# Optimization experiments

Measured on AMD Instinct MI355X. Metric: run time of the kernel, lower is better.

The kernel has to match this reference:

```python
import jax, jax.numpy as jnp
import numpy as np

B, S, F = 256, 512, 26
H, M, C = 512, 256, 20  # rnn_hidden, mlp_hidden, num_classes


def setup_inputs() -> dict:
    key = jax.random.key(0)
    ks = jax.random.split(key, 9)
    s_ih = 1.0 / np.sqrt(H)
    return {
        "x": jax.random.normal(ks[0], (B, S, F), dtype=jnp.float32),
        "w_ih": jax.random.uniform(ks[1], (4 * H, F), jnp.float32, -s_ih, s_ih),
        "w_hh": jax.random.uniform(ks[2], (4 * H, H), jnp.float32, -s_ih, s_ih),
        "b_ih": jax.random.uniform(ks[3], (4 * H,), jnp.float32, -s_ih, s_ih),
        "b_hh": jax.random.uniform(ks[4], (4 * H,), jnp.float32, -s_ih, s_ih),
        "w1": jax.random.uniform(ks[5], (M, H), jnp.float32, -s_ih, s_ih),
        "b1": jax.random.uniform(ks[6], (M,), jnp.float32, -s_ih, s_ih),
        "w2": jax.random.uniform(ks[7], (C, M), jnp.float32, -1.0 / np.sqrt(M), 1.0 / np.sqrt(M)),
        "b2": jax.random.uniform(ks[8], (C,), jnp.float32, -1.0 / np.sqrt(M), 1.0 / np.sqrt(M)),
    }


def reference(x, w_ih, w_hh, b_ih, b_hh, w1, b1, w2, b2):
    b, s, _ = x.shape
    h0 = jnp.zeros((b, H), x.dtype)
    c0 = jnp.zeros((b, H), x.dtype)
    bias = b_ih + b_hh

    def step(carry, xt):
        h, c = carry
        # original stores hx.data -> state carried into next step is detached
        h = jax.lax.stop_gradient(h)
        c = jax.lax.stop_gradient(c)
        z = xt @ w_ih.T + h @ w_hh.T + bias  # [b, 4H]
        i, f, g, o = jnp.split(z, 4, axis=-1)  # PyTorch gate order i,f,g,o
        c2 = jax.nn.sigmoid(f) * c + jax.nn.sigmoid(i) * jnp.tanh(g)
        h2 = jax.nn.sigmoid(o) * jnp.tanh(c2)
        return (h2, c2), h2

    _, hs = jax.lax.scan(step, (h0, c0), jnp.transpose(x, (1, 0, 2)))  # hs: [s, b, H]
    hs = jnp.transpose(hs, (1, 0, 2))  # [b, s, H]
    hidden = jax.nn.relu(jnp.einsum("bsh,mh->bsm", hs, w1) + b1)
    logits = jnp.einsum("bsm,cm->bsc", hidden, w2) + b2
    return jax.nn.log_softmax(logits, axis=-1)
```

## Files before the change

kernel.cpp:

```cpp
#include <hip/hip_runtime.h>

#define S_LEN 512
#define HID   512
#define FEAT  26
#define NCLS  20
#define DRING 16

typedef short bf16x8 __attribute__((ext_vector_type(8)));
typedef float f32x4  __attribute__((ext_vector_type(4)));

__device__ __forceinline__ unsigned short f2bf(float f) {
    unsigned u = __builtin_bit_cast(unsigned, f);
    unsigned r = (u + 0x7FFFu + ((u >> 16) & 1u)) >> 16;
    return (unsigned short)r;
}
__device__ __forceinline__ float sigm(float x) { return 1.f / (1.f + __expf(-x)); }
__device__ __forceinline__ float tanh_f(float x) {
    float xc = fminf(fmaxf(x, -15.f), 15.f);
    float t = __expf(-2.f * xc);
    return (1.f - t) / (1.f + t);
}

__device__ __forceinline__ void load4_coherent(const unsigned short* p,
                                               uint4& a0, uint4& a1, uint4& a2, uint4& a3) {
    asm volatile(
        "global_load_dwordx4 %0, %4, off sc0 sc1\n\t"
        "global_load_dwordx4 %1, %5, off sc0 sc1\n\t"
        "global_load_dwordx4 %2, %6, off sc0 sc1\n\t"
        "global_load_dwordx4 %3, %7, off sc0 sc1\n\t"
        "s_waitcnt vmcnt(0)"
        : "=&v"(a0), "=&v"(a1), "=&v"(a2), "=&v"(a3)
        : "v"(p), "v"(p + 8), "v"(p + 16), "v"(p + 24)
        : "memory");
}
__device__ __forceinline__ void store_coherent(unsigned short* p, unsigned d) {
    asm volatile(
        "global_store_dword %0, %1, off sc0 sc1\n\t"
        "s_waitcnt vmcnt(0)"
        :: "v"(p), "v"(d) : "memory");
}
__device__ __forceinline__ void store_coherent_x2(unsigned short* p, unsigned long long d) {
    asm volatile(
        "global_store_dwordx2 %0, %1, off sc0 sc1\n\t"
        "s_waitcnt vmcnt(0)"
        :: "v"(p), "v"(d) : "memory");
}
__device__ __forceinline__ void store_u32_nowait(unsigned* p, unsigned d) {
    asm volatile("global_store_dword %0, %1, off sc0 sc1" :: "v"(p), "v"(d) : "memory");
}
__device__ __forceinline__ unsigned load_u32_coherent(const unsigned* p) {
    unsigned v;
    asm volatile("global_load_dword %0, %1, off sc0 sc1\n\ts_waitcnt vmcnt(0)"
                 : "=v"(v) : "v"(p) : "memory");
    return v;
}

__global__ void prep_kernel(const float* __restrict__ w1, const float* __restrict__ w2,
                            unsigned short* __restrict__ w1b, unsigned short* __restrict__ w2b,
                            unsigned* __restrict__ syncw, int nclear) {
    int i = blockIdx.x * 256 + threadIdx.x;
    if (i < nclear) syncw[i] = 0u;
    if (i < 256 * 512) w1b[i] = f2bf(w1[i]);
    if (i < NCLS * 256) w2b[i] = f2bf(w2[i]);
}

__global__ __launch_bounds__(256, 1) void lstm_big_kernel(
    const float* __restrict__ x,
    const float* __restrict__ w_ih,
    const float* __restrict__ w_hh,
    const float* __restrict__ b_ih,
    const float* __restrict__ b_hh,
    const unsigned short* __restrict__ w1b,
    const float* __restrict__ b1,
    const unsigned short* __restrict__ w2b,
    const float* __restrict__ b2,
    float* __restrict__ out,
    unsigned short* __restrict__ hs,
    unsigned* __restrict__ flags)
{
    const int tid  = threadIdx.x;
    const int wave = tid >> 6;
    const int lane = tid & 63;
    const int quad = lane >> 4;
    const int l16  = lane & 15;
    const int wg   = blockIdx.x;

    __shared__ __align__(16) unsigned short At[16 * 552];
    __shared__ float zb[16 * 260];
    __shared__ __align__(16) unsigned short hid[16 * 264];
    __shared__ float lg[16 * 24];
    __shared__ unsigned rdy;
    if (tid == 0) rdy = 0u;
    __syncthreads();

    if (wg < 128) {
        const int clust = wg >> 3;
        const int wic   = wg & 7;
        const int B0    = clust * 16;
        const int U0    = wic * 64;

        bf16x8 bB[4][17];
#pragma unroll
        for (int tl = 0; tl < 4; ++tl) {
            const int row = wave * 512 + U0 + tl * 16 + l16;
            const float* wrow = w_hh + (size_t)row * HID;
#pragma unroll
            for (int kk = 0; kk < 16; ++kk) {
                const float* p = wrow + kk * 32 + quad * 8;
                bf16x8 v;
#pragma unroll
                for (int j = 0; j < 8; ++j) v[j] = (short)f2bf(p[j]);
                bB[tl][kk] = v;
            }
            const float* irow = w_ih + (size_t)row * FEAT;
            bf16x8 v;
#pragma unroll
            for (int j = 0; j < 8; ++j) {
                int ftr = quad * 8 + j;
                v[j] = (ftr < FEAT) ? (short)f2bf(irow[ftr]) : (short)0;
            }
            bB[tl][16] = v;
        }

        const int gb = tid >> 4;
        const int gu = tid & 15;
        float bias[4][4];
#pragma unroll
        for (int uu = 0; uu < 4; ++uu)
#pragma unroll
            for (int g = 0; g < 4; ++g) {
                int r = g * 512 + U0 + 4 * gu + uu;
                bias[uu][g] = b_ih[r] + b_hh[r];
            }
        float cst[4] = {0.f, 0.f, 0.f, 0.f};

        const int sm = tid >> 4;
        const int sc = tid & 15;
        unsigned short* hsc = hs + (size_t)clust * S_LEN * 16 * HID;
        unsigned* myflag = flags + (clust * 8 + wic) * 16;
        const unsigned* peer = flags + (clust * 8 + (lane & 7)) * 16;

        for (int t = 0; t < S_LEN; ++t) {
            {
                unsigned pk = 0u;
                if (sc <= 12) {
                    float2 xv = *(const float2*)(x + ((size_t)(B0 + sm) * S_LEN + t) * FEAT + sc * 2);
                    pk = (unsigned)f2bf(xv.x) | ((unsigned)f2bf(xv.y) << 16);
                }
                *(unsigned*)(At + sm * 552 + 512 + sc * 2) = pk;
            }
            if (t > 0) {
                if (wave == 0) {
                    for (;;) {
                        unsigned v = load_u32_coherent(peer);
                        if (__ballot(v >= (unsigned)t) == ~0ull) break;
                        __builtin_amdgcn_s_sleep(1);
                    }
                    if (lane == 0)
                        __hip_atomic_store(&rdy, (unsigned)t, __ATOMIC_RELAXED,
                                           __HIP_MEMORY_SCOPE_WORKGROUP);
                } else {
                    while (__hip_atomic_load(&rdy, __ATOMIC_RELAXED,
                                             __HIP_MEMORY_SCOPE_WORKGROUP) < (unsigned)t)
                        __builtin_amdgcn_s_sleep(1);
                }
                const unsigned short* src =
                    hsc + ((size_t)(t - 1) * 16 + sm) * HID + sc * 32;
                unsigned short* dst = At + sm * 552 + sc * 32;
                uint4 a0, a1, a2, a3;
                load4_coherent(src, a0, a1, a2, a3);
                *(uint4*)(dst)      = a0;
                *(uint4*)(dst + 8)  = a1;
                *(uint4*)(dst + 16) = a2;
                *(uint4*)(dst + 24) = a3;
            }
            __syncthreads();

            f32x4 acc[4];
#pragma unroll
            for (int tl = 0; tl < 4; ++tl) acc[tl] = (f32x4){0.f, 0.f, 0.f, 0.f};
            const unsigned short* arow = At + l16 * 552 + quad * 8;
            if (t > 0) {
#pragma unroll
                for (int kk = 0; kk < 17; ++kk) {
                    bf16x8 a = __builtin_bit_cast(bf16x8, *(const uint4*)(arow + kk * 32));
#pragma unroll
                    for (int tl = 0; tl < 4; ++tl)
                        acc[tl] = __builtin_amdgcn_mfma_f32_16x16x32_bf16(a, bB[tl][kk], acc[tl], 0, 0, 0);
                }
            } else {
                bf16x8 a = __builtin_bit_cast(bf16x8, *(const uint4*)(arow + 16 * 32));
#pragma unroll
                for (int tl = 0; tl < 4; ++tl)
                    acc[tl] = __builtin_amdgcn_mfma_f32_16x16x32_bf16(a, bB[tl][16], acc[tl], 0, 0, 0);
            }
#pragma unroll
            for (int tl = 0; tl < 4; ++tl)
#pragma unroll
                for (int r = 0; r < 4; ++r)
                    zb[(quad * 4 + r) * 260 + wave * 64 + tl * 16 + l16] = acc[tl][r];
            __syncthreads();

            {
                const float* zrow = zb + gb * 260;
                unsigned short hv[4];
#pragma unroll
                for (int uu = 0; uu < 4; ++uu) {
                    int u = 4 * gu + uu;
                    float zi = zrow[u]       + bias[uu][0];
                    float zf = zrow[64 + u]  + bias[uu][1];
                    float zg = zrow[128 + u] + bias[uu][2];
                    float zo = zrow[192 + u] + bias[uu][3];
                    float cn = sigm(zf) * cst[uu] + sigm(zi) * tanh_f(zg);
                    cst[uu] = cn;
                    hv[uu] = f2bf(sigm(zo) * tanh_f(cn));
                }
                unsigned long long d = (unsigned long long)hv[0]
                                     | ((unsigned long long)hv[1] << 16)
                                     | ((unsigned long long)hv[2] << 32)
                                     | ((unsigned long long)hv[3] << 48);
                unsigned short* hp = hsc + ((size_t)t * 16 + gb) * HID + U0 + 4 * gu;
                store_coherent_x2(hp, d);
            }
            __syncthreads();
            if (tid == 0) store_u32_nowait(myflag, (unsigned)(t + 1));
        }
    } else {
        const int mwg  = wg - 128;
        const int mc   = mwg >> 3;
        const int m    = mwg & 7;
        const int B0   = mc * 16;
        const unsigned* peer = flags + (mc * 8 + (lane & 7)) * 16;
        const unsigned short* hsc = hs + (size_t)mc * S_LEN * 16 * HID;
        const int sm = tid >> 4;
        const int sc = tid & 15;

        for (int t = m; t < S_LEN; t += 8) {
            if (wave == 0) {
                for (;;) {
                    unsigned v = load_u32_coherent(peer);
                    if (__ballot(v >= (unsigned)(t + 1)) == ~0ull) break;
                    __builtin_amdgcn_s_sleep(8);
                }
                if (lane == 0)
                    __hip_atomic_store(&rdy, (unsigned)(t + 1), __ATOMIC_RELAXED,
                                       __HIP_MEMORY_SCOPE_WORKGROUP);
            } else {
                while (__hip_atomic_load(&rdy, __ATOMIC_RELAXED,
                                         __HIP_MEMORY_SCOPE_WORKGROUP) < (unsigned)(t + 1))
                    __builtin_amdgcn_s_sleep(8);
            }
            {
                const unsigned short* src = hsc + ((size_t)t * 16 + sm) * HID + sc * 32;
                unsigned short* dst = At + sm * 552 + sc * 32;
                uint4 a0, a1, a2, a3;
                load4_coherent(src, a0, a1, a2, a3);
                *(uint4*)(dst)      = a0;
                *(uint4*)(dst + 8)  = a1;
                *(uint4*)(dst + 16) = a2;
                *(uint4*)(dst + 24) = a3;
            }
            __syncthreads();

            f32x4 a1[4];
#pragma unroll
            for (int nt = 0; nt < 4; ++nt) a1[nt] = (f32x4){0.f, 0.f, 0.f, 0.f};
#pragma unroll
            for (int kk = 0; kk < 16; ++kk) {
                bf16x8 a = __builtin_bit_cast(
                    bf16x8, *(const uint4*)(At + l16 * 552 + kk * 32 + quad * 8));
#pragma unroll
                for (int nt = 0; nt < 4; ++nt) {
                    int n = wave * 64 + nt * 16 + l16;
                    bf16x8 b = __builtin_bit_cast(
                        bf16x8, *(const uint4*)(w1b + (size_t)n * 512 + kk * 32 + quad * 8));
                    a1[nt] = __builtin_amdgcn_mfma_f32_16x16x32_bf16(a, b, a1[nt], 0, 0, 0);
                }
            }
#pragma unroll
            for (int nt = 0; nt < 4; ++nt) {
                int n = wave * 64 + nt * 16 + l16;
                float bv = b1[n];
#pragma unroll
                for (int r = 0; r < 4; ++r)
                    hid[(quad * 4 + r) * 264 + n] = f2bf(fmaxf(a1[nt][r] + bv, 0.f));
            }
            __syncthreads();
            if (wave == 0) {
                f32x4 a2[2];
                a2[0] = (f32x4){0.f, 0.f, 0.f, 0.f};
                a2[1] = (f32x4){0.f, 0.f, 0.f, 0.f};
#pragma unroll
                for (int kk = 0; kk < 8; ++kk) {
                    bf16x8 a = __builtin_bit_cast(
                        bf16x8, *(const uint4*)(hid + l16 * 264 + kk * 32 + quad * 8));
#pragma unroll
                    for (int nt = 0; nt < 2; ++nt) {
                        int n = nt * 16 + l16;
                        bf16x8 b;
                        if (n < NCLS) {
                            b = __builtin_bit_cast(
                                bf16x8, *(const uint4*)(w2b + (size_t)n * 256 + kk * 32 + quad * 8));
                        } else {
                            uint4 z; z.x = z.y = z.z = z.w = 0u;
                            b = __builtin_bit_cast(bf16x8, z);
                        }
                        a2[nt] = __builtin_amdgcn_mfma_f32_16x16x32_bf16(a, b, a2[nt], 0, 0, 0);
                    }
                }
#pragma unroll
                for (int nt = 0; nt < 2; ++nt) {
                    int n = nt * 16 + l16;
                    if (n < NCLS) {
                        float bv = b2[n];
#pragma unroll
                        for (int r = 0; r < 4; ++r)
                            lg[(quad * 4 + r) * 24 + n] = a2[nt][r] + bv;
                    }
                }
            }
            __syncthreads();
            if (tid < 16) {
                float v[NCLS];
                float mx = -3.4e38f;
#pragma unroll
                for (int c = 0; c < NCLS; ++c) { v[c] = lg[tid * 24 + c]; mx = fmaxf(mx, v[c]); }
                float s = 0.f;
#pragma unroll
                for (int c = 0; c < NCLS; ++c) s += __expf(v[c] - mx);
                float lse = mx + __logf(s);
                float* orow = out + ((size_t)(B0 + tid) * S_LEN + t) * NCLS;
#pragma unroll
                for (int c = 0; c < NCLS; ++c) orow[c] = v[c] - lse;
            }
            __syncthreads();
        }
    }
}

__global__ __launch_bounds__(256, 2) void lstm_fused_kernel(
    const float* __restrict__ x, const float* __restrict__ w_ih,
    const float* __restrict__ w_hh, const float* __restrict__ b_ih,
    const float* __restrict__ b_hh, const unsigned short* __restrict__ w1b,
    const float* __restrict__ b1, const unsigned short* __restrict__ w2b,
    const float* __restrict__ b2, float* __restrict__ out,
    unsigned short* __restrict__ hb, unsigned* __restrict__ flags,
    unsigned* __restrict__ done)
{
    const int tid  = threadIdx.x;
    const int wave = tid >> 6;
    const int lane = tid & 63;
    const int quad = lane >> 4;
    const int l16  = lane & 15;
    const int wg   = blockIdx.x;

    __shared__ __align__(16) unsigned short At[16 * 552];
    __shared__ float zb[16 * 132];
    __shared__ __align__(16) unsigned short hid[16 * 264];
    __shared__ float lg[16 * 24];
    __shared__ unsigned rdy;
    if (tid == 0) rdy = 0u;
    __syncthreads();

    if (wg < 256) {
        const int clust = (wg & 7) * 2 + (wg >= 128 ? 1 : 0);
        const int wic   = (wg >> 3) & 15;
        const int B0    = clust * 16;
        const int U0    = wic * 32;

        bf16x8 bB[2][17];
#pragma unroll
        for (int tl = 0; tl < 2; ++tl) {
            const int row = wave * 512 + U0 + tl * 16 + l16;
            const float* wrow = w_hh + (size_t)row * HID;
#pragma unroll
            for (int kk = 0; kk < 16; ++kk) {
                const float* p = wrow + kk * 32 + quad * 8;
                bf16x8 v;
#pragma unroll
                for (int j = 0; j < 8; ++j) v[j] = (short)f2bf(p[j]);
                bB[tl][kk] = v;
            }
            const float* irow = w_ih + (size_t)row * FEAT;
            bf16x8 v;
#pragma unroll
            for (int j = 0; j < 8; ++j) {
                int ftr = quad * 8 + j;
                v[j] = (ftr < FEAT) ? (short)f2bf(irow[ftr]) : (short)0;
            }
            bB[tl][16] = v;
        }

        const int gb = tid >> 4;
        const int gu = tid & 15;
        float bias[2][4];
#pragma unroll
        for (int uu = 0; uu < 2; ++uu)
#pragma unroll
            for (int g = 0; g < 4; ++g) {
                int r = g * 512 + U0 + 2 * gu + uu;
                bias[uu][g] = b_ih[r] + b_hh[r];
            }
        float cst[2] = {0.f, 0.f};

        const int sm = tid >> 4;
        const int sc = tid & 15;
        unsigned short* hbc = hb + (size_t)clust * DRING * 16 * HID;
        unsigned* myflag = flags + (clust * 16 + wic) * 16;
        const unsigned* peer = flags + (clust * 16 + (lane & 15)) * 16;

        for (int t = 0; t < S_LEN; ++t) {
            {
                unsigned pk = 0u;
                if (sc <= 12) {
                    float2 xv = *(const float2*)(x + ((size_t)(B0 + sm) * S_LEN + t) * FEAT + sc * 2);
                    pk = (unsigned)f2bf(xv.x) | ((unsigned)f2bf(xv.y) << 16);
                }
                *(unsigned*)(At + sm * 552 + 512 + sc * 2) = pk;
            }
            if (t > 0) {
                if (wave == 0) {
                    if (t >= DRING && lane == 0) {
                        const unsigned* dn = done + (clust * 8 + (t & 7)) * 16;
                        while (load_u32_coherent(dn) < (unsigned)(t - (DRING - 1)))
                            __builtin_amdgcn_s_sleep(8);
                    }
                    for (;;) {
                        unsigned v = load_u32_coherent(peer);
                        if (__ballot(v >= (unsigned)t) == ~0ull) break;
                        __builtin_amdgcn_s_sleep(1);
                    }
                    if (lane == 0)
                        __hip_atomic_store(&rdy, (unsigned)t, __ATOMIC_RELAXED,
                                           __HIP_MEMORY_SCOPE_WORKGROUP);
                } else {
                    while (__hip_atomic_load(&rdy, __ATOMIC_RELAXED,
                                             __HIP_MEMORY_SCOPE_WORKGROUP) < (unsigned)t)
                        __builtin_amdgcn_s_sleep(1);
                }
                const unsigned short* src =
                    hbc + ((t - 1) & (DRING - 1)) * 16 * HID + sm * HID + sc * 32;
                unsigned short* dst = At + sm * 552 + sc * 32;
                uint4 a0, a1, a2, a3;
                load4_coherent(src, a0, a1, a2, a3);
                *(uint4*)(dst)      = a0;
                *(uint4*)(dst + 8)  = a1;
                *(uint4*)(dst + 16) = a2;
                *(uint4*)(dst + 24) = a3;
            }
            __syncthreads();

            f32x4 acc0 = {0.f, 0.f, 0.f, 0.f};
            f32x4 acc1 = {0.f, 0.f, 0.f, 0.f};
            const unsigned short* arow = At + l16 * 552 + quad * 8;
            if (t > 0) {
#pragma unroll
                for (int kk = 0; kk < 17; ++kk) {
                    bf16x8 a = __builtin_bit_cast(bf16x8, *(const uint4*)(arow + kk * 32));
                    acc0 = __builtin_amdgcn_mfma_f32_16x16x32_bf16(a, bB[0][kk], acc0, 0, 0, 0);
                    acc1 = __builtin_amdgcn_mfma_f32_16x16x32_bf16(a, bB[1][kk], acc1, 0, 0, 0);
                }
            } else {
                bf16x8 a = __builtin_bit_cast(bf16x8, *(const uint4*)(arow + 16 * 32));
                acc0 = __builtin_amdgcn_mfma_f32_16x16x32_bf16(a, bB[0][16], acc0, 0, 0, 0);
                acc1 = __builtin_amdgcn_mfma_f32_16x16x32_bf16(a, bB[1][16], acc1, 0, 0, 0);
            }
#pragma unroll
            for (int r = 0; r < 4; ++r) {
                zb[(quad * 4 + r) * 132 + wave * 32 + l16]      = acc0[r];
                zb[(quad * 4 + r) * 132 + wave * 32 + 16 + l16] = acc1[r];
            }
            __syncthreads();

            {
                const float* zrow = zb + gb * 132;
                unsigned short hv2[2];
#pragma unroll
                for (int uu = 0; uu < 2; ++uu) {
                    int u = 2 * gu + uu;
                    float zi = zrow[u]      + bias[uu][0];
                    float zf = zrow[32 + u] + bias[uu][1];
                    float zg = zrow[64 + u] + bias[uu][2];
                    float zo = zrow[96 + u] + bias[uu][3];
                    float cn = sigm(zf) * cst[uu] + sigm(zi) * tanh_f(zg);
                    cst[uu] = cn;
                    hv2[uu] = f2bf(sigm(zo) * tanh_f(cn));
                }
                unsigned short* hp =
                    hbc + (t & (DRING - 1)) * 16 * HID + gb * HID + U0 + 2 * gu;
                store_coherent(hp, (unsigned)hv2[0] | ((unsigned)hv2[1] << 16));
            }
            __syncthreads();
            if (tid == 0) store_u32_nowait(myflag, (unsigned)(t + 1));
        }
    } else {
        const int mwg  = wg - 256;
        const int mc   = mwg >> 3;
        const int m    = mwg & 7;
        const int B0   = mc * 16;
        unsigned* mydone = done + (mc * 8 + m) * 16;
        const unsigned* peer = flags + (mc * 16 + (lane & 15)) * 16;
        const unsigned short* hbc = hb + (size_t)mc * DRING * 16 * HID;
        const int sm = tid >> 4;
        const int sc = tid & 15;

        for (int t = m; t < S_LEN; t += 8) {
            if (wave == 0) {
                for (;;) {
                    unsigned v = load_u32_coherent(peer);
                    if (__ballot(v >= (unsigned)(t + 1)) == ~0ull) break;
                    __builtin_amdgcn_s_sleep(8);
                }
                if (lane == 0)
                    __hip_atomic_store(&rdy, (unsigned)(t + 1), __ATOMIC_RELAXED,
                                       __HIP_MEMORY_SCOPE_WORKGROUP);
            } else {
                while (__hip_atomic_load(&rdy, __ATOMIC_RELAXED,
                                         __HIP_MEMORY_SCOPE_WORKGROUP) < (unsigned)(t + 1))
                    __builtin_amdgcn_s_sleep(8);
            }
            {
                const unsigned short* src =
                    hbc + (t & (DRING - 1)) * 16 * HID + sm * HID + sc * 32;
                unsigned short* dst = At + sm * 552 + sc * 32;
                uint4 a0, a1, a2, a3;
                load4_coherent(src, a0, a1, a2, a3);
                *(uint4*)(dst)      = a0;
                *(uint4*)(dst + 8)  = a1;
                *(uint4*)(dst + 16) = a2;
                *(uint4*)(dst + 24) = a3;
            }
            __syncthreads();
            if (tid == 0) store_u32_nowait(mydone, (unsigned)(t + 1));

            f32x4 a1[4];
#pragma unroll
            for (int nt = 0; nt < 4; ++nt) a1[nt] = (f32x4){0.f, 0.f, 0.f, 0.f};
#pragma unroll
            for (int kk = 0; kk < 16; ++kk) {
                bf16x8 a = __builtin_bit_cast(
                    bf16x8, *(const uint4*)(At + l16 * 552 + kk * 32 + quad * 8));
#pragma unroll
                for (int nt = 0; nt < 4; ++nt) {
                    int n = wave * 64 + nt * 16 + l16;
                    bf16x8 b = __builtin_bit_cast(
                        bf16x8, *(const uint4*)(w1b + (size_t)n * 512 + kk * 32 + quad * 8));
                    a1[nt] = __builtin_amdgcn_mfma_f32_16x16x32_bf16(a, b, a1[nt], 0, 0, 0);
                }
            }
#pragma unroll
            for (int nt = 0; nt < 4; ++nt) {
                int n = wave * 64 + nt * 16 + l16;
                float bv = b1[n];
#pragma unroll
                for (int r = 0; r < 4; ++r)
                    hid[(quad * 4 + r) * 264 + n] = f2bf(fmaxf(a1[nt][r] + bv, 0.f));
            }
            __syncthreads();
            if (wave == 0) {
                f32x4 a2[2];
                a2[0] = (f32x4){0.f, 0.f, 0.f, 0.f};
                a2[1] = (f32x4){0.f, 0.f, 0.f, 0.f};
#pragma unroll
                for (int kk = 0; kk < 8; ++kk) {
                    bf16x8 a = __builtin_bit_cast(
                        bf16x8, *(const uint4*)(hid + l16 * 264 + kk * 32 + quad * 8));
#pragma unroll
                    for (int nt = 0; nt < 2; ++nt) {
                        int n = nt * 16 + l16;
                        bf16x8 b;
                        if (n < NCLS) {
                            b = __builtin_bit_cast(
                                bf16x8, *(const uint4*)(w2b + (size_t)n * 256 + kk * 32 + quad * 8));
                        } else {
                            uint4 z; z.x = z.y = z.z = z.w = 0u;
                            b = __builtin_bit_cast(bf16x8, z);
                        }
                        a2[nt] = __builtin_amdgcn_mfma_f32_16x16x32_bf16(a, b, a2[nt], 0, 0, 0);
                    }
                }
#pragma unroll
                for (int nt = 0; nt < 2; ++nt) {
                    int n = nt * 16 + l16;
                    if (n < NCLS) {
                        float bv = b2[n];
#pragma unroll
                        for (int r = 0; r < 4; ++r)
                            lg[(quad * 4 + r) * 24 + n] = a2[nt][r] + bv;
                    }
                }
            }
            __syncthreads();
            if (tid < 16) {
                float v[NCLS];
                float mx = -3.4e38f;
#pragma unroll
                for (int c = 0; c < NCLS; ++c) { v[c] = lg[tid * 24 + c]; mx = fmaxf(mx, v[c]); }
                float s = 0.f;
#pragma unroll
                for (int c = 0; c < NCLS; ++c) s += __expf(v[c] - mx);
                float lse = mx + __logf(s);
                float* orow = out + ((size_t)(B0 + tid) * S_LEN + t) * NCLS;
#pragma unroll
                for (int c = 0; c < NCLS; ++c) orow[c] = v[c] - lse;
            }
            __syncthreads();
        }
    }
}

extern "C" void kernel_launch(void* const* d_in, const int* in_sizes, int n_in,
                              void* d_out, int out_size, void* d_ws, size_t ws_size,
                              hipStream_t stream) {
    const float* x    = (const float*)d_in[0];
    const float* w_ih = (const float*)d_in[1];
    const float* w_hh = (const float*)d_in[2];
    const float* b_ih = (const float*)d_in[3];
    const float* b_hh = (const float*)d_in[4];
    const float* w1   = (const float*)d_in[5];
    const float* b1   = (const float*)d_in[6];
    const float* w2   = (const float*)d_in[7];
    const float* b2   = (const float*)d_in[8];
    char* ws = (char*)d_ws;

    const size_t HS_BYTES = (size_t)16 * S_LEN * 16 * HID * 2;
    const size_t NEED_BIG = HS_BYTES + 8192 + 262144 + 10240;

    if (ws_size >= NEED_BIG) {
        unsigned short* hsb   = (unsigned short*)ws;
        unsigned*       flags = (unsigned*)(ws + HS_BYTES);
        unsigned short* w1b   = (unsigned short*)(ws + HS_BYTES + 8192);
        unsigned short* w2b   = (unsigned short*)(ws + HS_BYTES + 8192 + 262144);
        prep_kernel<<<512, 256, 0, stream>>>(w1, w2, w1b, w2b, flags, 2048);
        lstm_big_kernel<<<256, 256, 0, stream>>>(x, w_ih, w_hh, b_ih, b_hh,
                                                 w1b, b1, w2b, b2,
                                                 (float*)d_out, hsb, flags);
    } else {
        unsigned short* hb    = (unsigned short*)ws;
        unsigned*       flags = (unsigned*)(ws + 4194304);
        unsigned*       done  = (unsigned*)(ws + 4194304 + 16384);
        unsigned short* w1b   = (unsigned short*)(ws + 4194304 + 16384 + 8192);
        unsigned short* w2b   = (unsigned short*)(ws + 4194304 + 16384 + 8192 + 262144);
        prep_kernel<<<512, 256, 0, stream>>>(w1, w2, w1b, w2b, flags, 6144);
        lstm_fused_kernel<<<384, 256, 0, stream>>>(x, w_ih, w_hh, b_ih, b_hh,
                                                   w1b, b1, w2b, b2,
                                                   (float*)d_out, hb, flags, done);
    }
}
```

Measured before the change: 2.101 ms.

## Map clusters to one XCD and use L2-scope coherence when co-located

Remaps block indices so that each batch cluster's LSTM and MLP workgroups are meant to land on the same XCD, assuming round-robin dispatch by blockIdx modulo 8. At startup each workgroup reads its XCC_ID and publishes it in the flag area. If every member of a cluster reports the same XCC, the per-step hidden-state exchange and flag polling switch from system-scope (sc0 sc1) to device-scope (sc0) loads and stores, which the author intends to be served from the shared L2 instead of going past it. This targets the latency of the serial cross-workgroup handoff on every timestep. It adds a startup handshake and relies on the dispatch-order assumption, with a fallback to the old coherent path when members sit on different XCDs.

```diff
diff --git a/kernel.cpp b/kernel.cpp
--- a/kernel.cpp
+++ b/kernel.cpp
@@ -51,6 +51,38 @@
 __device__ __forceinline__ unsigned load_u32_coherent(const unsigned* p) {
     unsigned v;
     asm volatile("global_load_dword %0, %1, off sc0 sc1\n\ts_waitcnt vmcnt(0)"
+                 : "=v"(v) : "v"(p) : "memory");
+    return v;
+}
+__device__ __forceinline__ void store_u32_sys_wait(unsigned* p, unsigned d) {
+    asm volatile("global_store_dword %0, %1, off sc0 sc1\n\ts_waitcnt vmcnt(0)"
+                 :: "v"(p), "v"(d) : "memory");
+}
+
+__device__ __forceinline__ void load4_l2(const unsigned short* p,
+                                         uint4& a0, uint4& a1, uint4& a2, uint4& a3) {
+    asm volatile(
+        "global_load_dwordx4 %0, %4, off sc0\n\t"
+        "global_load_dwordx4 %1, %5, off sc0\n\t"
+        "global_load_dwordx4 %2, %6, off sc0\n\t"
+        "global_load_dwordx4 %3, %7, off sc0\n\t"
+        "s_waitcnt vmcnt(0)"
+        : "=&v"(a0), "=&v"(a1), "=&v"(a2), "=&v"(a3)
+        : "v"(p), "v"(p + 8), "v"(p + 16), "v"(p + 24)
+        : "memory");
+}
+__device__ __forceinline__ void store_l2_x2(unsigned short* p, unsigned long long d) {
+    asm volatile(
+        "global_store_dwordx2 %0, %1, off sc0\n\t"
+        "s_waitcnt vmcnt(0)"
+        :: "v"(p), "v"(d) : "memory");
+}
+__device__ __forceinline__ void store_u32_nowait_l2(unsigned* p, unsigned d) {
+    asm volatile("global_store_dword %0, %1, off sc0" :: "v"(p), "v"(d) : "memory");
+}
+__device__ __forceinline__ unsigned load_u32_l2(const unsigned* p) {
+    unsigned v;
+    asm volatile("global_load_dword %0, %1, off sc0\n\ts_waitcnt vmcnt(0)"
                  : "=v"(v) : "v"(p) : "memory");
     return v;
 }
@@ -83,21 +115,51 @@
     const int lane = tid & 63;
     const int quad = lane >> 4;
     const int l16  = lane & 15;
-    const int wg   = blockIdx.x;
+
+    const int  bx      = blockIdx.x;
+    const int  xasm    = bx & 7;
+    const int  kslt    = bx >> 3;
+    const bool is_lstm = (kslt < 16);
+    const int  ksub    = is_lstm ? kslt : (kslt - 16);
+    const int  clust   = xasm * 2 + (ksub >> 3);
+    const int  sub     = ksub & 7;
 
     __shared__ __align__(16) unsigned short At[16 * 552];
     __shared__ float zb[16 * 260];
     __shared__ __align__(16) unsigned short hid[16 * 264];
     __shared__ float lg[16 * 24];
     __shared__ unsigned rdy;
+    __shared__ unsigned fastf;
     if (tid == 0) rdy = 0u;
+
+    {
+        unsigned xcc;
+        asm volatile("s_getreg_b32 %0, hwreg(HW_REG_XCC_ID)" : "=s"(xcc));
+        if (tid == 0) {
+            unsigned* slot = flags + (clust * 8 + sub) * 16 + (is_lstm ? 8 : 9);
+            store_u32_sys_wait(slot, (xcc & 0xFu) + 1u);
+        }
+        if (wave == 0) {
+            const unsigned* ps = flags + (clust * 8 + (lane & 7)) * 16 + ((lane & 8) ? 9 : 8);
+            unsigned myx = 1u;
+            for (;;) {
+                unsigned v = 1u;
+                if (lane < 16) v = load_u32_coherent(ps);
+                if (__ballot(v != 0u) == ~0ull) { myx = v; break; }
+                __builtin_amdgcn_s_sleep(2);
+            }
+            unsigned ref = __shfl(myx, 0);
+            bool eq = (lane >= 16) || (myx == ref);
+            if (tid == 0) fastf = (__ballot(eq) == ~0ull) ? 1u : 0u;
+        }
+    }
     __syncthreads();
-
-    if (wg < 128) {
-        const int clust = wg >> 3;
-        const int wic   = wg & 7;
-        const int B0    = clust * 16;
-        const int U0    = wic * 64;
+    const bool fast = (fastf != 0u);
+
+    if (is_lstm) {
+        const int wic = sub;
+        const int B0  = clust * 16;
+        const int U0  = wic * 64;
 
         bf16x8 bB[4][17];
 #pragma unroll
@@ -152,7 +214,7 @@
             if (t > 0) {
                 if (wave == 0) {
                     for (;;) {
-                        unsigned v = load_u32_coherent(peer);
+                        unsigned v = fast ? load_u32_l2(peer) : load_u32_coherent(peer);
                         if (__ballot(v >= (unsigned)t) == ~0ull) break;
                         __builtin_amdgcn_s_sleep(1);
                     }
@@ -168,7 +230,8 @@
                     hsc + ((size_t)(t - 1) * 16 + sm) * HID + sc * 32;
                 unsigned short* dst = At + sm * 552 + sc * 32;
                 uint4 a0, a1, a2, a3;
-                load4_coherent(src, a0, a1, a2, a3);
+                if (fast) load4_l2(src, a0, a1, a2, a3);
+                else      load4_coherent(src, a0, a1, a2, a3);
                 *(uint4*)(dst)      = a0;
                 *(uint4*)(dst + 8)  = a1;
                 *(uint4*)(dst + 16) = a2;
@@ -220,16 +283,19 @@
                                      | ((unsigned long long)hv[2] << 32)
                                      | ((unsigned long long)hv[3] << 48);
                 unsigned short* hp = hsc + ((size_t)t * 16 + gb) * HID + U0 + 4 * gu;
-                store_coherent_x2(hp, d);
-            }
-            __syncthreads();
-            if (tid == 0) store_u32_nowait(myflag, (unsigned)(t + 1));
+                if (fast) store_l2_x2(hp, d);
+                else      store_coherent_x2(hp, d);
+            }
+            __syncthreads();
+            if (tid == 0) {
+                if (fast) store_u32_nowait_l2(myflag, (unsigned)(t + 1));
+                else      store_u32_nowait(myflag, (unsigned)(t + 1));
+            }
         }
     } else {
-        const int mwg  = wg - 128;
-        const int mc   = mwg >> 3;
-        const int m    = mwg & 7;
-        const int B0   = mc * 16;
+        const int mc  = clust;
+        const int m   = sub;
+        const int B0  = mc * 16;
         const unsigned* peer = flags + (mc * 8 + (lane & 7)) * 16;
         const unsigned short* hsc = hs + (size_t)mc * S_LEN * 16 * HID;
         const int sm = tid >> 4;
@@ -238,7 +304,7 @@
         for (int t = m; t < S_LEN; t += 8) {
             if (wave == 0) {
                 for (;;) {
-                    unsigned v = load_u32_coherent(peer);
+                    unsigned v = fast ? load_u32_l2(peer) : load_u32_coherent(peer);
                     if (__ballot(v >= (unsigned)(t + 1)) == ~0ull) break;
                     __builtin_amdgcn_s_sleep(8);
                 }
@@ -254,7 +320,8 @@
                 const unsigned short* src = hsc + ((size_t)t * 16 + sm) * HID + sc * 32;
                 unsigned short* dst = At + sm * 552 + sc * 32;
                 uint4 a0, a1, a2, a3;
-                load4_coherent(src, a0, a1, a2, a3);
+                if (fast) load4_l2(src, a0, a1, a2, a3);
+                else      load4_coherent(src, a0, a1, a2, a3);
                 *(uint4*)(dst)      = a0;
                 *(uint4*)(dst + 8)  = a1;
                 *(uint4*)(dst + 16) = a2;
```

Result: no change. 2.073 ms (-1.3%).
